# Optimization experiments

Measured on AMD Instinct MI355X. Metric: run time of the kernel, lower is better.

The kernel has to match this reference:

```python
import jax, jax.numpy as jnp
import numpy as np

HIDDEN = 51
OUT = 2

def setup_inputs() -> dict:
    key = jax.random.key(0)
    ks = jax.random.split(key, 7)
    B, T = 1024, 8192
    inp = jax.random.normal(ks[0], (B, T), dtype=jnp.float32)
    s_ih = 1.0 / np.sqrt(HIDDEN)
    W_ih = jax.random.uniform(ks[1], (4 * HIDDEN, 1), jnp.float32, -s_ih, s_ih)
    W_hh = jax.random.uniform(ks[2], (4 * HIDDEN, HIDDEN), jnp.float32, -s_ih, s_ih)
    b_ih = jax.random.uniform(ks[3], (4 * HIDDEN,), jnp.float32, -s_ih, s_ih)
    b_hh = jax.random.uniform(ks[4], (4 * HIDDEN,), jnp.float32, -s_ih, s_ih)
    W_lin = jax.random.uniform(ks[5], (OUT, HIDDEN), jnp.float32, -s_ih, s_ih)
    b_lin = jax.random.uniform(ks[6], (OUT,), jnp.float32, -s_ih, s_ih)
    return {"input": inp, "W_ih": W_ih, "W_hh": W_hh, "b_ih": b_ih,
            "b_hh": b_hh, "W_lin": W_lin, "b_lin": b_lin}

def reference(input, W_ih, W_hh, b_ih, b_hh, W_lin, b_lin):
    B, T = input.shape
    # Precompute input-to-gate projections for all steps: [T, B, 4H]
    x_proj = input.T[:, :, None] * W_ih[:, 0][None, None, :] + b_ih + b_hh

    def step(carry, x_g):
        h, c = carry
        gates = x_g + h @ W_hh.T  # [B, 4H]
        i, f, g, o = jnp.split(gates, 4, axis=-1)
        i, f, o = jax.nn.sigmoid(i), jax.nn.sigmoid(f), jax.nn.sigmoid(o)
        g = jnp.tanh(g)
        c = f * c + i * g
        h = o * jnp.tanh(c)
        out = h @ W_lin.T + b_lin  # [B, 2]
        return (h, c), out

    h0 = jnp.zeros((B, HIDDEN), dtype=input.dtype)
    c0 = jnp.zeros((B, HIDDEN), dtype=input.dtype)
    _, outs = jax.lax.scan(step, (h0, c0), x_proj)  # outs: [T, B, 2]
    return jnp.transpose(outs, (1, 2, 0))  # [B, 2, T]
```

## Files before the change

kernel.cpp:

```cpp
#include <hip/hip_runtime.h>

#define H 51
#define T_LEN 8192
#define CHUNK 64

__device__ __forceinline__ float fast_sigmoid(float x) {
    float e = __builtin_amdgcn_exp2f(x * -1.44269504088896341f);
    return __builtin_amdgcn_rcpf(1.0f + e);
}

__device__ __forceinline__ float fast_tanh(float x) {
    float e = __builtin_amdgcn_exp2f(x * -2.88539008177792681f);
    float r = __builtin_amdgcn_rcpf(1.0f + e);
    return fmaf(2.0f, r, -1.0f);
}

__device__ __forceinline__ float bcast_lane(float v, int lane) {
    return __int_as_float(__builtin_amdgcn_readlane(__float_as_int(v), lane));
}

template <int CTRL, int RM>
__device__ __forceinline__ float dpp_add(float v) {
    int t = __builtin_amdgcn_update_dpp(0, __float_as_int(v), CTRL, RM, 0xF, false);
    return v + __int_as_float(t);
}
__device__ __forceinline__ float wave_sum_to_lane63(float v) {
    v = dpp_add<0x111, 0xF>(v);
    v = dpp_add<0x112, 0xF>(v);
    v = dpp_add<0x114, 0xF>(v);
    v = dpp_add<0x118, 0xF>(v);
    v = dpp_add<0x142, 0xA>(v);
    v = dpp_add<0x143, 0xC>(v);
    return v;
}

extern "C" __global__ void __launch_bounds__(64, 1)
lstm_fused(const float* __restrict__ input,
           const float* __restrict__ W_ih,
           const float* __restrict__ W_hh,
           const float* __restrict__ b_ih,
           const float* __restrict__ b_hh,
           const float* __restrict__ W_lin,
           const float* __restrict__ b_lin,
           float* __restrict__ out)
{
    const int L = threadIdx.x;
    const int b = blockIdx.x;
    const bool act = (L < H);

    float w[4][H];
#pragma unroll
    for (int g = 0; g < 4; ++g) {
#pragma unroll
        for (int k = 0; k < H; ++k) {
            w[g][k] = act ? W_hh[(g * H + L) * H + k] : 0.0f;
        }
    }
    float wi[4], bsum[4];
#pragma unroll
    for (int g = 0; g < 4; ++g) {
        wi[g]   = act ? W_ih[g * H + L] : 0.0f;
        bsum[g] = act ? (b_ih[g * H + L] + b_hh[g * H + L]) : 0.0f;
    }
    const float wl0 = act ? W_lin[L]     : 0.0f;
    const float wl1 = act ? W_lin[H + L] : 0.0f;
    const float bl0 = b_lin[0];
    const float bl1 = b_lin[1];

    float h = 0.0f, c = 0.0f;

    const float* inrow = input + (size_t)b * T_LEN;
    float* out0 = out + (size_t)b * 2 * T_LEN;
    float* out1 = out0 + T_LEN;

    float x_cur = inrow[L];

    for (int t0 = 0; t0 < T_LEN; t0 += CHUNK) {
        float x_next = 0.0f;
        if (t0 + CHUNK < T_LEN) x_next = inrow[t0 + CHUNK + L];
        float v0 = 0.0f, v1 = 0.0f;

#pragma unroll 2
        for (int k = 0; k < CHUNK; ++k) {
            const float xk = bcast_lane(x_cur, k);

            float acc0 = fmaf(xk, wi[0], bsum[0]);
            float acc1 = fmaf(xk, wi[1], bsum[1]);
            float acc2 = fmaf(xk, wi[2], bsum[2]);
            float acc3 = fmaf(xk, wi[3], bsum[3]);
#pragma unroll
            for (int kk = 0; kk < H; ++kk) {
                const float hk = bcast_lane(h, kk);
                acc0 = fmaf(hk, w[0][kk], acc0);
                acc1 = fmaf(hk, w[1][kk], acc1);
                acc2 = fmaf(hk, w[2][kk], acc2);
                acc3 = fmaf(hk, w[3][kk], acc3);
            }

            const float ig = fast_sigmoid(acc0);
            const float fg = fast_sigmoid(acc1);
            const float gg = fast_tanh(acc2);
            const float og = fast_sigmoid(acc3);
            c = fmaf(fg, c, ig * gg);
            h = og * fast_tanh(c);

            float p0 = wave_sum_to_lane63(h * wl0);
            float p1 = wave_sum_to_lane63(h * wl1);
            const float s0 = bcast_lane(p0, 63);
            const float s1 = bcast_lane(p1, 63);
            if (k == L) { v0 = s0 + bl0; v1 = s1 + bl1; }
        }

        out0[t0 + L] = v0;
        out1[t0 + L] = v1;
        x_cur = x_next;
    }
}

extern "C" void kernel_launch(void* const* d_in, const int* in_sizes, int n_in,
                              void* d_out, int out_size, void* d_ws, size_t ws_size,
                              hipStream_t stream) {
    const float* input = (const float*)d_in[0];
    const float* W_ih  = (const float*)d_in[1];
    const float* W_hh  = (const float*)d_in[2];
    const float* b_ih  = (const float*)d_in[3];
    const float* b_hh  = (const float*)d_in[4];
    const float* W_lin = (const float*)d_in[5];
    const float* b_lin = (const float*)d_in[6];
    float* outp = (float*)d_out;

    const int B = in_sizes[0] / T_LEN;
    lstm_fused<<<dim3(B), dim3(64), 0, stream>>>(
        input, W_ih, W_hh, b_ih, b_hh, W_lin, b_lin, outp);
}
```

Before: 4.852 ms.

## Defer output projection to per-chunk LDS pass instead of per-step wave reductions

After: 6.078 ms. 1.25x slower.

```diff
diff --git a/kernel.cpp b/kernel.cpp
--- a/kernel.cpp
+++ b/kernel.cpp
@@ -3,6 +3,7 @@
 #define H 51
 #define T_LEN 8192
 #define CHUNK 64
+#define ROWP 53
 
 __device__ __forceinline__ float fast_sigmoid(float x) {
     float e = __builtin_amdgcn_exp2f(x * -1.44269504088896341f);
@@ -19,22 +20,9 @@
     return __int_as_float(__builtin_amdgcn_readlane(__float_as_int(v), lane));
 }
 
-template <int CTRL, int RM>
-__device__ __forceinline__ float dpp_add(float v) {
-    int t = __builtin_amdgcn_update_dpp(0, __float_as_int(v), CTRL, RM, 0xF, false);
-    return v + __int_as_float(t);
-}
-__device__ __forceinline__ float wave_sum_to_lane63(float v) {
-    v = dpp_add<0x111, 0xF>(v);
-    v = dpp_add<0x112, 0xF>(v);
-    v = dpp_add<0x114, 0xF>(v);
-    v = dpp_add<0x118, 0xF>(v);
-    v = dpp_add<0x142, 0xA>(v);
-    v = dpp_add<0x143, 0xC>(v);
-    return v;
-}
-
-extern "C" __global__ void __launch_bounds__(64, 1)
+extern "C" __global__ void
+__launch_bounds__(64)
+__attribute__((amdgpu_waves_per_eu(1, 1)))
 lstm_fused(const float* __restrict__ input,
            const float* __restrict__ W_ih,
            const float* __restrict__ W_hh,
@@ -47,6 +35,8 @@
     const int L = threadIdx.x;
     const int b = blockIdx.x;
     const bool act = (L < H);
+
+    __shared__ __align__(16) float sh[CHUNK * ROWP];
 
     float w[4][H];
 #pragma unroll
@@ -62,8 +52,15 @@
         wi[g]   = act ? W_ih[g * H + L] : 0.0f;
         bsum[g] = act ? (b_ih[g * H + L] + b_hh[g * H + L]) : 0.0f;
     }
-    const float wl0 = act ? W_lin[L]     : 0.0f;
-    const float wl1 = act ? W_lin[H + L] : 0.0f;
+#pragma unroll
+    for (int g = 0; g < 4; ++g) {
+#pragma unroll
+        for (int k = 0; k < H; ++k) {
+            asm volatile("" : "+v"(w[g][k]));
+        }
+        asm volatile("" : "+v"(wi[g]), "+v"(bsum[g]));
+    }
+
     const float bl0 = b_lin[0];
     const float bl1 = b_lin[1];
 
@@ -78,9 +75,7 @@
     for (int t0 = 0; t0 < T_LEN; t0 += CHUNK) {
         float x_next = 0.0f;
         if (t0 + CHUNK < T_LEN) x_next = inrow[t0 + CHUNK + L];
-        float v0 = 0.0f, v1 = 0.0f;
 
-#pragma unroll 2
         for (int k = 0; k < CHUNK; ++k) {
             const float xk = bcast_lane(x_cur, k);
 
@@ -104,15 +99,23 @@
             c = fmaf(fg, c, ig * gg);
             h = og * fast_tanh(c);
 
-            float p0 = wave_sum_to_lane63(h * wl0);
-            float p1 = wave_sum_to_lane63(h * wl1);
-            const float s0 = bcast_lane(p0, 63);
-            const float s1 = bcast_lane(p1, 63);
-            if (k == L) { v0 = s0 + bl0; v1 = s1 + bl1; }
+            sh[k * ROWP + L] = h;
         }
 
-        out0[t0 + L] = v0;
-        out1[t0 + L] = v1;
+        __syncthreads();
+
+        float o0 = bl0, o1 = bl1;
+        const float* hr = &sh[L * ROWP];
+#pragma unroll
+        for (int kk = 0; kk < H; ++kk) {
+            const float hk = hr[kk];
+            o0 = fmaf(hk, W_lin[kk],     o0);
+            o1 = fmaf(hk, W_lin[H + kk], o1);
+        }
+        out0[t0 + L] = o0;
+        out1[t0 + L] = o1;
+
+        __syncthreads();
         x_cur = x_next;
     }
 }
```
